# Optimization experiments

Hardware: AMD Instinct MI355X
Metric: run time of the kernel (lower is better)

## Reference

```python
import jax, jax.numpy as jnp
import numpy as np

B, V = 1024, 4096
CHUNK = 16  # rows of x per cdist chunk; bounds intermediate to CHUNK*B*V floats (~268MB)
T = 2.0      # module hardcodes self.T = 2 regardless of init arg
EPS = 0.1
N_ITERS = 20


def _cdist_l1(x, y):
    # torch.cdist(x, y, p=1): out[i, j] = sum_v |x[i, v] - y[j, v]| -> [B, B]
    # chunk over rows of x to avoid materializing [B, B, V]
    xc = x.reshape(B // CHUNK, CHUNK, V)
    f = lambda xb: jnp.sum(jnp.abs(xb[:, None, :] - y[None, :, :]), axis=-1)  # [CHUNK, B]
    return jax.lax.map(f, xc).reshape(B, B)


def setup_inputs() -> dict:
    key = jax.random.key(0)
    k1, k2 = jax.random.split(key)
    y_s = jax.random.normal(k1, (B, V), dtype=jnp.float32)
    y_t = jax.random.normal(k2, (B, V), dtype=jnp.float32)
    return {"y_s": y_s, "y_t": y_t}


def reference(y_s, y_t):
    p_s = jax.nn.softmax(y_s / T, axis=1)
    p_t = jax.nn.softmax(y_t / T, axis=1)
    Wxy = _cdist_l1(p_s, p_t)          # [B, B] L1 cost matrix
    K = jnp.exp(-Wxy / EPS)

    def body(P, _):
        P = P / jnp.sum(P, axis=1, keepdims=True)  # row normalize
        P = P / jnp.sum(P, axis=0, keepdims=True)  # col normalize
        return P, None

    P, _ = jax.lax.scan(body, K, None, length=N_ITERS)
    return 0.001 * jnp.sum(P * Wxy)
```

## Files before the change

kernel.cpp:

```cpp
#include <hip/hip_runtime.h>
#include <hip/hip_fp16.h>

#define BSZ 1024
#define VSZ 4096
#define NBLK 32
#define JPB 32
#define KPAD 1040

__global__ __launch_bounds__(256) void softmax_kernel(const float* __restrict__ ys,
                                                      const float* __restrict__ yt,
                                                      unsigned short* __restrict__ ps,
                                                      unsigned short* __restrict__ pt) {
    int row = blockIdx.x;
    const float* src;
    unsigned short* dst;
    if (row < BSZ) { src = ys + (size_t)row * VSZ;         dst = ps + (size_t)row * VSZ; }
    else           { src = yt + (size_t)(row - BSZ) * VSZ; dst = pt + (size_t)(row - BSZ) * VSZ; }
    int t = threadIdx.x;
    float4 v[4];
    float m = -1e30f;
#pragma unroll
    for (int k = 0; k < 4; ++k) {
        v[k] = ((const float4*)src)[t + 256 * k];
        m = fmaxf(m, fmaxf(fmaxf(v[k].x, v[k].y), fmaxf(v[k].z, v[k].w)));
    }
#pragma unroll
    for (int d = 32; d >= 1; d >>= 1) m = fmaxf(m, __shfl_down(m, d));
    __shared__ float sred[4];
    __shared__ float sred2[4];
    int lane = t & 63, wid = t >> 6;
    if (lane == 0) sred[wid] = m;
    __syncthreads();
    m = fmaxf(fmaxf(sred[0], sred[1]), fmaxf(sred[2], sred[3]));
    const float C = 0.7213475204444817f;
    float s = 0.f;
#pragma unroll
    for (int k = 0; k < 4; ++k) {
        v[k].x = exp2f((v[k].x - m) * C);
        v[k].y = exp2f((v[k].y - m) * C);
        v[k].z = exp2f((v[k].z - m) * C);
        v[k].w = exp2f((v[k].w - m) * C);
        s += (v[k].x + v[k].y) + (v[k].z + v[k].w);
    }
#pragma unroll
    for (int d = 32; d >= 1; d >>= 1) s += __shfl_down(s, d);
    if (lane == 0) sred2[wid] = s;
    __syncthreads();
    s = (sred2[0] + sred2[1]) + (sred2[2] + sred2[3]);
    float inv = 65535.0f / s;
#pragma unroll
    for (int k = 0; k < 4; ++k) {
        union { unsigned short h[4]; uint2 u; } o;
        o.h[0] = (unsigned short)__float2uint_rn(fminf(v[k].x * inv, 65535.0f));
        o.h[1] = (unsigned short)__float2uint_rn(fminf(v[k].y * inv, 65535.0f));
        o.h[2] = (unsigned short)__float2uint_rn(fminf(v[k].z * inv, 65535.0f));
        o.h[3] = (unsigned short)__float2uint_rn(fminf(v[k].w * inv, 65535.0f));
        ((uint2*)dst)[t + 256 * k] = o.u;
    }
}

#define TSI 128
#define TSJ 64
#define LSTR 72

__global__ __launch_bounds__(256, 4) void cdist_kernel(const unsigned short* __restrict__ psh,
                                                       const unsigned short* __restrict__ pth,
                                                       float* __restrict__ spart) {
    __shared__ unsigned short sP[TSI * LSTR];
    __shared__ unsigned short sQ[TSJ * LSTR];
    const int bi = blockIdx.x;
    const int bj = blockIdx.y;
    const int bv = blockIdx.z;
    const int t = threadIdx.x;
    const int cl = t & 15;
    const int rl = t >> 4;

    const int pr = t >> 1, pc = (t & 1) * 32;
    const int qr = t >> 2, qc = (t & 3) * 16;
    const unsigned short* gP = psh + (size_t)(bi * TSI + pr) * VSZ + bv * 1024 + pc;
    const unsigned short* gQ = pth + (size_t)(bj * TSJ + qr) * VSZ + bv * 1024 + qc;
    unsigned short* lP = &sP[pr * LSTR + pc];
    unsigned short* lQ = &sQ[qr * LSTR + qc];

    unsigned acc[4][8];
#pragma unroll
    for (int w = 0; w < 4; ++w)
#pragma unroll
        for (int u = 0; u < 8; ++u) acc[w][u] = 0u;

    for (int kt = 0; kt < 16; ++kt) {
        const unsigned short* gp = gP + kt * 64;
        const unsigned short* gq = gQ + kt * 64;
        uint4 a0 = *(const uint4*)(gp + 0);
        uint4 a1 = *(const uint4*)(gp + 8);
        uint4 a2 = *(const uint4*)(gp + 16);
        uint4 a3 = *(const uint4*)(gp + 24);
        uint4 b0 = *(const uint4*)(gq + 0);
        uint4 b1 = *(const uint4*)(gq + 8);
        __syncthreads();
        *(uint4*)(lP + 0)  = a0;
        *(uint4*)(lP + 8)  = a1;
        *(uint4*)(lP + 16) = a2;
        *(uint4*)(lP + 24) = a3;
        *(uint4*)(lQ + 0)  = b0;
        *(uint4*)(lQ + 8)  = b1;
        __syncthreads();
        const unsigned short* pbase = sP + cl * LSTR;
        const unsigned short* qbase = sQ + rl * LSTR;
#pragma unroll
        for (int vv = 0; vv < 8; ++vv) {
            uint4 q[4];
#pragma unroll
            for (int w = 0; w < 4; ++w)
                q[w] = *(const uint4*)(qbase + w * 16 * LSTR + vv * 8);
#pragma unroll
            for (int h = 0; h < 4; ++h) {
                uint4 p0 = *(const uint4*)(pbase + (2 * h + 0) * 16 * LSTR + vv * 8);
                uint4 p1 = *(const uint4*)(pbase + (2 * h + 1) * 16 * LSTR + vv * 8);
#pragma unroll
                for (int w = 0; w < 4; ++w) {
                    unsigned a = acc[w][2 * h + 0];
                    a = __builtin_amdgcn_sad_u16(p0.x, q[w].x, a);
                    a = __builtin_amdgcn_sad_u16(p0.y, q[w].y, a);
                    a = __builtin_amdgcn_sad_u16(p0.z, q[w].z, a);
                    a = __builtin_amdgcn_sad_u16(p0.w, q[w].w, a);
                    acc[w][2 * h + 0] = a;
                    unsigned b = acc[w][2 * h + 1];
                    b = __builtin_amdgcn_sad_u16(p1.x, q[w].x, b);
                    b = __builtin_amdgcn_sad_u16(p1.y, q[w].y, b);
                    b = __builtin_amdgcn_sad_u16(p1.z, q[w].z, b);
                    b = __builtin_amdgcn_sad_u16(p1.w, q[w].w, b);
                    acc[w][2 * h + 1] = b;
                }
            }
        }
    }

    float* outp = spart + (size_t)bv * (BSZ * BSZ);
    const float SCL = 1.0f / 65535.0f;
#pragma unroll
    for (int w = 0; w < 4; ++w) {
        size_t jr = (size_t)(bj * TSJ + rl + 16 * w);
#pragma unroll
        for (int u = 0; u < 8; ++u) {
            int ic = bi * TSI + cl + 16 * u;
            outp[jr * BSZ + ic] = (float)acc[w][u] * SCL;
        }
    }
}

__global__ __launch_bounds__(256) void combine_kernel(const float* __restrict__ spart,
                                                      float* __restrict__ wt,
                                                      float* __restrict__ kt,
                                                      float* __restrict__ cpart,
                                                      unsigned* __restrict__ flags) {
    if (blockIdx.x == 0 && threadIdx.x < NBLK) flags[threadIdx.x * 32] = 0u;
    if (blockIdx.x < 3) {
        float4 z4; z4.x = z4.y = z4.z = z4.w = 0.f;
        ((float4*)cpart)[blockIdx.x * 256 + threadIdx.x] = z4;
    }
    int idx = blockIdx.x * 256 + threadIdx.x;
    const float4* p0 = (const float4*)spart;
    const int Q = (BSZ * BSZ) / 4;
    float4 a = p0[idx], b = p0[idx + Q], c = p0[idx + 2 * Q], d = p0[idx + 3 * Q];
    float4 w;
    w.x = (a.x + b.x) + (c.x + d.x);
    w.y = (a.y + b.y) + (c.y + d.y);
    w.z = (a.z + b.z) + (c.z + d.z);
    w.w = (a.w + b.w) + (c.w + d.w);
    ((float4*)wt)[idx] = w;
    const float CE = -14.426950408889634f;
    float4 k;
    k.x = exp2f(w.x * CE);
    k.y = exp2f(w.y * CE);
    k.z = exp2f(w.z * CE);
    k.w = exp2f(w.w * CE);
    ((float4*)kt)[idx] = k;
}

__device__ inline void grid_barrier(unsigned* flags, unsigned gen) {
    __syncthreads();
    const int t = threadIdx.x;
    if (t == 0)
        __hip_atomic_store(&flags[blockIdx.x * 32], gen, __ATOMIC_RELEASE, __HIP_MEMORY_SCOPE_AGENT);
    if (t < NBLK) {
        while (__hip_atomic_load(&flags[t * 32], __ATOMIC_RELAXED, __HIP_MEMORY_SCOPE_AGENT) < gen)
            __builtin_amdgcn_s_sleep(1);
    }
    __syncthreads();
    if (t == 0)
        (void)__hip_atomic_load(&flags[0], __ATOMIC_ACQUIRE, __HIP_MEMORY_SCOPE_AGENT);
    __syncthreads();
}

__global__ __launch_bounds__(512) void sinkhorn_kernel(const float* __restrict__ KT,
                                                       const float* __restrict__ WT,
                                                       float* __restrict__ cpart,
                                                       float* __restrict__ outpart,
                                                       float* __restrict__ out,
                                                       unsigned* __restrict__ flags) {
    __shared__ __align__(16) float k_lds[JPB * KPAD];
    __shared__ __align__(16) float a_sh[BSZ];
    __shared__ float b_sh[JPB];
    __shared__ float red[JPB];
    const int z = blockIdx.x;
    const int t = threadIdx.x;
    const int j0 = z * JPB;
#pragma unroll
    for (int m = 0; m < 16; ++m) {
        int idx = t + 512 * m;
        int row = idx >> 8;
        int col = (idx & 255) * 4;
        float4 v = *(const float4*)(KT + (size_t)(j0 + row) * BSZ + col);
        *(float4*)(&k_lds[row * KPAD + col]) = v;
    }
    if (t < JPB) b_sh[t] = 1.0f;
    __syncthreads();
    const int jj = t >> 4;
    const int il = t & 15;
    unsigned gen = 1u;
    for (int it = 0; it < 20; ++it) {
        float* cbuf = cpart + (size_t)(it % 3) * BSZ;
        float2 s = {0.f, 0.f};
#pragma unroll
        for (int q = 0; q < JPB; ++q) {
            float2 kv = *(const float2*)(&k_lds[q * KPAD + 2 * t]);
            float bb = b_sh[q];
            s.x += kv.x * bb; s.y += kv.y * bb;
        }
        (void)__hip_atomic_fetch_add(&cbuf[2 * t],     s.x, __ATOMIC_RELAXED, __HIP_MEMORY_SCOPE_AGENT);
        (void)__hip_atomic_fetch_add(&cbuf[2 * t + 1], s.y, __ATOMIC_RELAXED, __HIP_MEMORY_SCOPE_AGENT);
        grid_barrier(flags, gen++);
        float2 cv = *(const float2*)(&cbuf[2 * t]);
        if (t < 32) cpart[(size_t)((it + 2) % 3) * BSZ + z * 32 + t] = 0.f;
        float2 ar;
        ar.x = 1.0f / cv.x; ar.y = 1.0f / cv.y;
        ((float2*)a_sh)[t] = ar;
        __syncthreads();
        float sb = 0.f;
#pragma unroll
        for (int m2 = 0; m2 < 16; ++m2) {
            float4 kv = *(const float4*)(&k_lds[jj * KPAD + (il + 16 * m2) * 4]);
            float4 av = ((const float4*)a_sh)[il + 16 * m2];
            sb += (kv.x * av.x + kv.y * av.y) + (kv.z * av.z + kv.w * av.w);
        }
#pragma unroll
        for (int d = 8; d >= 1; d >>= 1) sb += __shfl_down(sb, d, 16);
        if (il == 0) b_sh[jj] = 1.0f / sb;
        __syncthreads();
    }
    {
        const float4* wrow = (const float4*)(WT + (size_t)(j0 + jj) * BSZ);
        float sb = 0.f;
#pragma unroll 4
        for (int m2 = 0; m2 < 16; ++m2) {
            float4 kv = *(const float4*)(&k_lds[jj * KPAD + (il + 16 * m2) * 4]);
            float4 wv = wrow[il + 16 * m2];
            float4 av = ((const float4*)a_sh)[il + 16 * m2];
            sb += (av.x * kv.x * wv.x + av.y * kv.y * wv.y) +
                  (av.z * kv.z * wv.z + av.w * kv.w * wv.w);
        }
#pragma unroll
        for (int d = 8; d >= 1; d >>= 1) sb += __shfl_down(sb, d, 16);
        if (il == 0) red[jj] = sb * b_sh[jj];
        __syncthreads();
        if (t == 0) {
            float ss = 0.f;
#pragma unroll
            for (int q = 0; q < JPB; ++q) ss += red[q];
            outpart[z] = ss;
        }
    }
    grid_barrier(flags, gen++);
    if (z == 0 && t == 0) {
        float ss = 0.f;
        for (int q = 0; q < NBLK; ++q) ss += outpart[q];
        out[0] = 0.001f * ss;
    }
}

extern "C" void kernel_launch(void* const* d_in, const int* in_sizes, int n_in,
                              void* d_out, int out_size, void* d_ws, size_t ws_size,
                              hipStream_t stream) {
    const float* ys = (const float*)d_in[0];
    const float* yt = (const float*)d_in[1];
    float* ws = (float*)d_ws;
    unsigned short* psh = (unsigned short*)ws;
    unsigned short* pth = (unsigned short*)(ws + 2ull * 1024 * 1024);
    float* spart   = ws + 4ull * 1024 * 1024;
    float* wt      = spart + 4ull * BSZ * BSZ;
    float* kt      = wt + (size_t)BSZ * BSZ;
    float* cpart   = kt + (size_t)BSZ * BSZ;
    float* outpart = cpart + 2ull * NBLK * BSZ;
    unsigned* flags = (unsigned*)(outpart + 128);
    float* outp    = (float*)d_out;

    softmax_kernel<<<dim3(2 * BSZ), dim3(256), 0, stream>>>(ys, yt, psh, pth);
    cdist_kernel<<<dim3(8, 16, 4), dim3(256), 0, stream>>>(psh, pth, spart);
    combine_kernel<<<dim3((BSZ * BSZ / 4) / 256), dim3(256), 0, stream>>>(spart, wt, kt, cpart, flags);

    void* args[] = {(void*)&kt, (void*)&wt, (void*)&cpart, (void*)&outpart, (void*)&outp,
                    (void*)&flags};
    (void)hipLaunchCooperativeKernel((void*)sinkhorn_kernel, dim3(NBLK), dim3(512), args, 0, stream);
}
```

Baseline: 284.8 us.

## Enlarge cdist tile with register prefetch, fuse exp into sinkhorn, stagger atomics

The cdist kernel tile grows to 128x128 with 8x8 accumulators per thread. It now prefetches the next K-slice into registers while computing on the current shared-memory tile, to hide global load latency, and launch bounds drop to 1 block per CU. The exp of the cost matrix moves from the combine kernel into the sinkhorn kernel's LDS load, which removes one full B×B write and read. Sinkhorn column atomics are rotated per block so blocks do not hit the same addresses together. The larger tile raises register pressure and halves the cdist grid to 256 blocks, which may lower occupancy.

```diff
diff --git a/kernel.cpp b/kernel.cpp
--- a/kernel.cpp
+++ b/kernel.cpp
@@ -60,10 +60,10 @@
 }
 
 #define TSI 128
-#define TSJ 64
+#define TSJ 128
 #define LSTR 72
 
-__global__ __launch_bounds__(256, 4) void cdist_kernel(const unsigned short* __restrict__ psh,
+__global__ __launch_bounds__(256, 1) void cdist_kernel(const unsigned short* __restrict__ psh,
                                                        const unsigned short* __restrict__ pth,
                                                        float* __restrict__ spart) {
     __shared__ unsigned short sP[TSI * LSTR];
@@ -75,50 +75,66 @@
     const int cl = t & 15;
     const int rl = t >> 4;
 
-    const int pr = t >> 1, pc = (t & 1) * 32;
-    const int qr = t >> 2, qc = (t & 3) * 16;
-    const unsigned short* gP = psh + (size_t)(bi * TSI + pr) * VSZ + bv * 1024 + pc;
-    const unsigned short* gQ = pth + (size_t)(bj * TSJ + qr) * VSZ + bv * 1024 + qc;
-    unsigned short* lP = &sP[pr * LSTR + pc];
-    unsigned short* lQ = &sQ[qr * LSTR + qc];
-
-    unsigned acc[4][8];
-#pragma unroll
-    for (int w = 0; w < 4; ++w)
+    const int sr = t >> 1, sc = (t & 1) * 32;
+    const unsigned short* gP = psh + (size_t)(bi * TSI + sr) * VSZ + bv * 1024 + sc;
+    const unsigned short* gQ = pth + (size_t)(bj * TSJ + sr) * VSZ + bv * 1024 + sc;
+    unsigned short* lP = &sP[sr * LSTR + sc];
+    unsigned short* lQ = &sQ[sr * LSTR + sc];
+
+    unsigned acc[8][8];
+#pragma unroll
+    for (int w = 0; w < 8; ++w)
 #pragma unroll
         for (int u = 0; u < 8; ++u) acc[w][u] = 0u;
 
-    for (int kt = 0; kt < 16; ++kt) {
-        const unsigned short* gp = gP + kt * 64;
-        const unsigned short* gq = gQ + kt * 64;
-        uint4 a0 = *(const uint4*)(gp + 0);
-        uint4 a1 = *(const uint4*)(gp + 8);
-        uint4 a2 = *(const uint4*)(gp + 16);
-        uint4 a3 = *(const uint4*)(gp + 24);
-        uint4 b0 = *(const uint4*)(gq + 0);
-        uint4 b1 = *(const uint4*)(gq + 8);
-        __syncthreads();
+    {
+        uint4 a0 = *(const uint4*)(gP + 0);
+        uint4 a1 = *(const uint4*)(gP + 8);
+        uint4 a2 = *(const uint4*)(gP + 16);
+        uint4 a3 = *(const uint4*)(gP + 24);
+        uint4 b0 = *(const uint4*)(gQ + 0);
+        uint4 b1 = *(const uint4*)(gQ + 8);
+        uint4 b2 = *(const uint4*)(gQ + 16);
+        uint4 b3 = *(const uint4*)(gQ + 24);
         *(uint4*)(lP + 0)  = a0;
         *(uint4*)(lP + 8)  = a1;
         *(uint4*)(lP + 16) = a2;
         *(uint4*)(lP + 24) = a3;
         *(uint4*)(lQ + 0)  = b0;
         *(uint4*)(lQ + 8)  = b1;
-        __syncthreads();
+        *(uint4*)(lQ + 16) = b2;
+        *(uint4*)(lQ + 24) = b3;
+    }
+    __syncthreads();
+
+    for (int kt = 0; kt < 16; ++kt) {
+        uint4 ra0, ra1, ra2, ra3, rb0, rb1, rb2, rb3;
+        if (kt < 15) {
+            const unsigned short* gp = gP + (kt + 1) * 64;
+            const unsigned short* gq = gQ + (kt + 1) * 64;
+            ra0 = *(const uint4*)(gp + 0);
+            ra1 = *(const uint4*)(gp + 8);
+            ra2 = *(const uint4*)(gp + 16);
+            ra3 = *(const uint4*)(gp + 24);
+            rb0 = *(const uint4*)(gq + 0);
+            rb1 = *(const uint4*)(gq + 8);
+            rb2 = *(const uint4*)(gq + 16);
+            rb3 = *(const uint4*)(gq + 24);
+        }
         const unsigned short* pbase = sP + cl * LSTR;
         const unsigned short* qbase = sQ + rl * LSTR;
 #pragma unroll
         for (int vv = 0; vv < 8; ++vv) {
-            uint4 q[4];
-#pragma unroll
-            for (int w = 0; w < 4; ++w)
+            uint4 q[8];
+#pragma unroll
+            for (int w = 0; w < 8; ++w)
                 q[w] = *(const uint4*)(qbase + w * 16 * LSTR + vv * 8);
 #pragma unroll
             for (int h = 0; h < 4; ++h) {
                 uint4 p0 = *(const uint4*)(pbase + (2 * h + 0) * 16 * LSTR + vv * 8);
                 uint4 p1 = *(const uint4*)(pbase + (2 * h + 1) * 16 * LSTR + vv * 8);
 #pragma unroll
-                for (int w = 0; w < 4; ++w) {
+                for (int w = 0; w < 8; ++w) {
                     unsigned a = acc[w][2 * h + 0];
                     a = __builtin_amdgcn_sad_u16(p0.x, q[w].x, a);
                     a = __builtin_amdgcn_sad_u16(p0.y, q[w].y, a);
@@ -134,12 +150,24 @@
                 }
             }
         }
+        if (kt < 15) {
+            __syncthreads();
+            *(uint4*)(lP + 0)  = ra0;
+            *(uint4*)(lP + 8)  = ra1;
+            *(uint4*)(lP + 16) = ra2;
+            *(uint4*)(lP + 24) = ra3;
+            *(uint4*)(lQ + 0)  = rb0;
+            *(uint4*)(lQ + 8)  = rb1;
+            *(uint4*)(lQ + 16) = rb2;
+            *(uint4*)(lQ + 24) = rb3;
+            __syncthreads();
+        }
     }
 
     float* outp = spart + (size_t)bv * (BSZ * BSZ);
     const float SCL = 1.0f / 65535.0f;
 #pragma unroll
-    for (int w = 0; w < 4; ++w) {
+    for (int w = 0; w < 8; ++w) {
         size_t jr = (size_t)(bj * TSJ + rl + 16 * w);
 #pragma unroll
         for (int u = 0; u < 8; ++u) {
@@ -151,7 +179,6 @@
 
 __global__ __launch_bounds__(256) void combine_kernel(const float* __restrict__ spart,
                                                       float* __restrict__ wt,
-                                                      float* __restrict__ kt,
                                                       float* __restrict__ cpart,
                                                       unsigned* __restrict__ flags) {
     if (blockIdx.x == 0 && threadIdx.x < NBLK) flags[threadIdx.x * 32] = 0u;
@@ -169,13 +196,6 @@
     w.z = (a.z + b.z) + (c.z + d.z);
     w.w = (a.w + b.w) + (c.w + d.w);
     ((float4*)wt)[idx] = w;
-    const float CE = -14.426950408889634f;
-    float4 k;
-    k.x = exp2f(w.x * CE);
-    k.y = exp2f(w.y * CE);
-    k.z = exp2f(w.z * CE);
-    k.w = exp2f(w.w * CE);
-    ((float4*)kt)[idx] = k;
 }
 
 __device__ inline void grid_barrier(unsigned* flags, unsigned gen) {
@@ -193,8 +213,7 @@
     __syncthreads();
 }
 
-__global__ __launch_bounds__(512) void sinkhorn_kernel(const float* __restrict__ KT,
-                                                       const float* __restrict__ WT,
+__global__ __launch_bounds__(512) void sinkhorn_kernel(const float* __restrict__ WT,
                                                        float* __restrict__ cpart,
                                                        float* __restrict__ outpart,
                                                        float* __restrict__ out,
@@ -206,36 +225,43 @@
     const int z = blockIdx.x;
     const int t = threadIdx.x;
     const int j0 = z * JPB;
+    const float CE = -14.426950408889634f;
 #pragma unroll
     for (int m = 0; m < 16; ++m) {
         int idx = t + 512 * m;
         int row = idx >> 8;
         int col = (idx & 255) * 4;
-        float4 v = *(const float4*)(KT + (size_t)(j0 + row) * BSZ + col);
-        *(float4*)(&k_lds[row * KPAD + col]) = v;
+        float4 w = *(const float4*)(WT + (size_t)(j0 + row) * BSZ + col);
+        float4 k;
+        k.x = exp2f(w.x * CE);
+        k.y = exp2f(w.y * CE);
+        k.z = exp2f(w.z * CE);
+        k.w = exp2f(w.w * CE);
+        *(float4*)(&k_lds[row * KPAD + col]) = k;
     }
     if (t < JPB) b_sh[t] = 1.0f;
     __syncthreads();
     const int jj = t >> 4;
     const int il = t & 15;
+    const int colp = (t + z * 16) & 511;
     unsigned gen = 1u;
     for (int it = 0; it < 20; ++it) {
         float* cbuf = cpart + (size_t)(it % 3) * BSZ;
         float2 s = {0.f, 0.f};
 #pragma unroll
         for (int q = 0; q < JPB; ++q) {
-            float2 kv = *(const float2*)(&k_lds[q * KPAD + 2 * t]);
+            float2 kv = *(const float2*)(&k_lds[q * KPAD + 2 * colp]);
             float bb = b_sh[q];
             s.x += kv.x * bb; s.y += kv.y * bb;
         }
-        (void)__hip_atomic_fetch_add(&cbuf[2 * t],     s.x, __ATOMIC_RELAXED, __HIP_MEMORY_SCOPE_AGENT);
-        (void)__hip_atomic_fetch_add(&cbuf[2 * t + 1], s.y, __ATOMIC_RELAXED, __HIP_MEMORY_SCOPE_AGENT);
+        (void)__hip_atomic_fetch_add(&cbuf[2 * colp],     s.x, __ATOMIC_RELAXED, __HIP_MEMORY_SCOPE_AGENT);
+        (void)__hip_atomic_fetch_add(&cbuf[2 * colp + 1], s.y, __ATOMIC_RELAXED, __HIP_MEMORY_SCOPE_AGENT);
         grid_barrier(flags, gen++);
-        float2 cv = *(const float2*)(&cbuf[2 * t]);
+        float2 cv = *(const float2*)(&cbuf[2 * colp]);
         if (t < 32) cpart[(size_t)((it + 2) % 3) * BSZ + z * 32 + t] = 0.f;
         float2 ar;
         ar.x = 1.0f / cv.x; ar.y = 1.0f / cv.y;
-        ((float2*)a_sh)[t] = ar;
+        ((float2*)a_sh)[colp] = ar;
         __syncthreads();
         float sb = 0.f;
 #pragma unroll
@@ -296,10 +322,9 @@
     float* outp    = (float*)d_out;
 
     softmax_kernel<<<dim3(2 * BSZ), dim3(256), 0, stream>>>(ys, yt, psh, pth);
-    cdist_kernel<<<dim3(8, 16, 4), dim3(256), 0, stream>>>(psh, pth, spart);
-    combine_kernel<<<dim3((BSZ * BSZ / 4) / 256), dim3(256), 0, stream>>>(spart, wt, kt, cpart, flags);
-
-    void* args[] = {(void*)&kt, (void*)&wt, (void*)&cpart, (void*)&outpart, (void*)&outp,
-                    (void*)&flags};
+    cdist_kernel<<<dim3(8, 8, 4), dim3(256), 0, stream>>>(psh, pth, spart);
+    combine_kernel<<<dim3((BSZ * BSZ / 4) / 256), dim3(256), 0, stream>>>(spart, wt, cpart, flags);
+
+    void* args[] = {(void*)&wt, (void*)&cpart, (void*)&outpart, (void*)&outp, (void*)&flags};
     (void)hipLaunchCooperativeKernel((void*)sinkhorn_kernel, dim3(NBLK), dim3(512), args, 0, stream);
 }
```

Result: slower. 518.7 us (+82.2%).
